# Optimization experiments

Measured on AMD Instinct MI355X. Metric: run time of the kernel, lower is better.

Reference implementation:

```python
import jax, jax.numpy as jnp
import numpy as np

B, N_MODES, N_CLASSES = 200000, 64, 10
HBAR = 2.0


def setup_inputs() -> dict:
    key = jax.random.key(0)
    k1, k2, k3, k4 = jax.random.split(key, 4)
    twoN = 2 * N_MODES
    x = jax.random.normal(k1, (B, N_MODES), dtype=jnp.float32)
    # Ansatz (learned Gaussian channel): symplectic-like matrix S and displacement d.
    S = jax.random.normal(k2, (twoN, twoN), dtype=jnp.float32) * (1.0 / np.sqrt(twoN))
    d = jax.random.normal(k3, (twoN,), dtype=jnp.float32)
    bias = jnp.zeros((N_MODES,), dtype=jnp.float32)
    W = jax.random.normal(k4, (N_CLASSES, N_MODES), dtype=jnp.float32) * (1.0 / np.sqrt(N_MODES))
    b = jnp.zeros((N_CLASSES,), dtype=jnp.float32)
    return {"x": x, "S": S, "d": d, "bias": bias, "W": W, "b": b}


def reference(x, S, d, bias, W, b):
    # Vacuum mean vector is zero; displacing mode i by alpha = x_i/sqrt(2*hbar)
    # shifts the x-quadrature (even indices, xpxp ordering) by sqrt(2*hbar)*Re(alpha) = x_i.
    Bn = x.shape[0]
    twoN = 2 * x.shape[1]
    mu = jnp.zeros((Bn, twoN), dtype=x.dtype).at[:, ::2].set(x)  # [B, 2N]
    # Ansatz: affine symplectic map mu' = S mu + d (cov transform S cov S^T does
    # not affect the expectation-value homodyne readout mu_x).
    mu_out = mu @ S.T + d  # [B, 2N]
    # Homodyne x-quadrature readout per mode + bias.
    readout = mu_out[:, ::2] + bias  # [B, N]
    return readout @ W.T + b  # [B, n_classes]
```

## Files before the change

kernel.cpp:

```cpp
#include <hip/hip_runtime.h>

#define NM 64
#define NC 10
#define TWO_N 128


__global__ __launch_bounds__(256) void cv2d_fused(
    const float* __restrict__ x,
    const float* __restrict__ S,
    const float* __restrict__ dvec,
    const float* __restrict__ bias,
    const float* __restrict__ W,
    const float* __restrict__ bvec,
    float* __restrict__ out,
    int Bn)
{
    __shared__ __align__(16) float Ms[NC][NM];
    __shared__ float c0s[NC];
    const int t = threadIdx.x;

    for (int e = t; e < NM * NC; e += 256) {
        const int c = e >> 6;
        const int m = e & 63;
        float acc = 0.f;
        #pragma unroll
        for (int k = 0; k < NM; ++k)
            acc += S[(2 * k) * TWO_N + 2 * m] * W[c * NM + k];
        Ms[c][m] = acc;
    }
    if (t < NC) {
        float acc = bvec[t];
        #pragma unroll
        for (int k = 0; k < NM; ++k)
            acc += (dvec[2 * k] + bias[k]) * W[t * NM + k];
        c0s[t] = acc;
    }
    __syncthreads();

    const int row = blockIdx.x * 256 + t;
    if (row >= Bn) return;

    const float4* __restrict__ xr = (const float4*)(x + (size_t)row * NM);

    float acc[NC];
    #pragma unroll
    for (int c = 0; c < NC; ++c) acc[c] = c0s[c];

    #pragma unroll
    for (int q = 0; q < NM / 4; ++q) {
        const float4 v = xr[q];
        #pragma unroll
        for (int c = 0; c < NC; ++c) {
            const float4 mm = *(const float4*)&Ms[c][4 * q];
            acc[c] += v.x * mm.x;
            acc[c] += v.y * mm.y;
            acc[c] += v.z * mm.z;
            acc[c] += v.w * mm.w;
        }
    }

    float2* __restrict__ o = (float2*)(out + (size_t)row * NC);
    #pragma unroll
    for (int c = 0; c < NC; c += 2)
        o[c / 2] = make_float2(acc[c], acc[c + 1]);
}

extern "C" void kernel_launch(void* const* d_in, const int* in_sizes, int n_in,
                              void* d_out, int out_size, void* d_ws, size_t ws_size,
                              hipStream_t stream) {
    const float* x    = (const float*)d_in[0];
    const float* S    = (const float*)d_in[1];
    const float* d    = (const float*)d_in[2];
    const float* bias = (const float*)d_in[3];
    const float* W    = (const float*)d_in[4];
    const float* bvec = (const float*)d_in[5];
    float* out = (float*)d_out;

    const int Bn = in_sizes[0] / NM;

    const int grid = (Bn + 255) / 256;
    cv2d_fused<<<grid, 256, 0, stream>>>(x, S, d, bias, W, bvec, out, Bn);
}
```

Measured before the change: 110.1 us.

## Precompute fused weight matrix in separate kernel and stage x via coalesced LDS loads

The per-block recomputation of the folded S·W matrix and constant term moves into a small pre-kernel that writes them to workspace, and the main kernel just copies them into shared memory. The main kernel also loads its tile of x with fully coalesced float4 reads into a padded shared-memory buffer, replacing the strided per-row float4 reads. Each thread then reads its row from LDS. This adds a second launch and a large LDS footprint (about 51KB per block), which may limit occupancy.

```diff
diff --git a/kernel.cpp b/kernel.cpp
--- a/kernel.cpp
+++ b/kernel.cpp
@@ -3,59 +3,81 @@
 #define NM 64
 #define NC 10
 #define TWO_N 128
+#define BT 192
+#define RS 67
 
 
-__global__ __launch_bounds__(256) void cv2d_fused(
+__global__ __launch_bounds__(64) void cv2d_pre(
+    const float* __restrict__ S, const float* __restrict__ dvec,
+    const float* __restrict__ bias, const float* __restrict__ W,
+    const float* __restrict__ bvec, float* __restrict__ MC)
+{
+    const int c = blockIdx.x, m = threadIdx.x;
+    if (c < NC) {
+        float acc = 0.f;
+        #pragma unroll
+        for (int k = 0; k < NM; ++k)
+            acc += S[(2 * k) * TWO_N + 2 * m] * W[c * NM + k];
+        MC[c * NM + m] = acc;
+    } else if (m < NC) {
+        float acc = bvec[m];
+        #pragma unroll
+        for (int k = 0; k < NM; ++k)
+            acc += (dvec[2 * k] + bias[k]) * W[m * NM + k];
+        MC[NC * NM + m] = acc;
+    }
+}
+
+__global__ __launch_bounds__(BT) void cv2d_main(
     const float* __restrict__ x,
-    const float* __restrict__ S,
-    const float* __restrict__ dvec,
-    const float* __restrict__ bias,
-    const float* __restrict__ W,
-    const float* __restrict__ bvec,
+    const float* __restrict__ MC,
     float* __restrict__ out,
     int Bn)
 {
+    __shared__ float xs[BT * RS];
     __shared__ __align__(16) float Ms[NC][NM];
     __shared__ float c0s[NC];
     const int t = threadIdx.x;
 
-    for (int e = t; e < NM * NC; e += 256) {
-        const int c = e >> 6;
-        const int m = e & 63;
-        float acc = 0.f;
-        #pragma unroll
-        for (int k = 0; k < NM; ++k)
-            acc += S[(2 * k) * TWO_N + 2 * m] * W[c * NM + k];
-        Ms[c][m] = acc;
+    for (int e = t; e < NC * NM; e += BT) ((float*)Ms)[e] = MC[e];
+    if (t < NC) c0s[t] = MC[NC * NM + t];
+
+    const long long f0 = (long long)blockIdx.x * (BT * 16) + t;
+    const long long fmax = (long long)Bn * 16;
+    const float4* __restrict__ xg = (const float4*)x;
+    float4 v[16];
+    #pragma unroll
+    for (int i = 0; i < 16; ++i) {
+        const long long f = f0 + BT * i;
+        v[i] = (f < fmax) ? xg[f] : make_float4(0.f, 0.f, 0.f, 0.f);
     }
-    if (t < NC) {
-        float acc = bvec[t];
-        #pragma unroll
-        for (int k = 0; k < NM; ++k)
-            acc += (dvec[2 * k] + bias[k]) * W[t * NM + k];
-        c0s[t] = acc;
+    const int r0 = t >> 4;
+    const int m0 = (t & 15) * 4;
+    #pragma unroll
+    for (int i = 0; i < 16; ++i) {
+        float* p = &xs[(r0 + 12 * i) * RS + m0];
+        p[0] = v[i].x; p[1] = v[i].y; p[2] = v[i].z; p[3] = v[i].w;
     }
     __syncthreads();
 
-    const int row = blockIdx.x * 256 + t;
+    const int row = blockIdx.x * BT + t;
     if (row >= Bn) return;
-
-    const float4* __restrict__ xr = (const float4*)(x + (size_t)row * NM);
 
     float acc[NC];
     #pragma unroll
     for (int c = 0; c < NC; ++c) acc[c] = c0s[c];
 
+    const float* __restrict__ xrow = &xs[t * RS];
     #pragma unroll
     for (int q = 0; q < NM / 4; ++q) {
-        const float4 v = xr[q];
+        const float a0 = xrow[4 * q + 0];
+        const float a1 = xrow[4 * q + 1];
+        const float a2 = xrow[4 * q + 2];
+        const float a3 = xrow[4 * q + 3];
         #pragma unroll
         for (int c = 0; c < NC; ++c) {
             const float4 mm = *(const float4*)&Ms[c][4 * q];
-            acc[c] += v.x * mm.x;
-            acc[c] += v.y * mm.y;
-            acc[c] += v.z * mm.z;
-            acc[c] += v.w * mm.w;
+            acc[c] += a0 * mm.x + a1 * mm.y + a2 * mm.z + a3 * mm.w;
         }
     }
 
@@ -75,9 +97,12 @@
     const float* W    = (const float*)d_in[4];
     const float* bvec = (const float*)d_in[5];
     float* out = (float*)d_out;
+    float* MC  = (float*)d_ws;
 
     const int Bn = in_sizes[0] / NM;
 
-    const int grid = (Bn + 255) / 256;
-    cv2d_fused<<<grid, 256, 0, stream>>>(x, S, d, bias, W, bvec, out, Bn);
+    cv2d_pre<<<NC + 1, 64, 0, stream>>>(S, d, bias, W, bvec, MC);
+
+    const int grid = (Bn + BT - 1) / BT;
+    cv2d_main<<<grid, BT, 0, stream>>>(x, MC, out, Bn);
 }
```

Measured after the change: 108.4 us. About the same (-1.6%).
